# Optimization experiments

Measured on AMD Instinct MI355X. Metric: run time of the kernel, lower is better.

Reference implementation:

```python
import jax, jax.numpy as jnp
import numpy as np

# Dims: B=1, S=2048, D=1024, L=4 blocks, INNER=2*D=2048, NH=4 heads (DH=512),
# conv K=4, qkv blocksize BS=4 (NB=512 block-diagonal blocks).

def _ln(x, w, eps=1e-5):
    mu = x.mean(-1, keepdims=True)
    var = x.var(-1, keepdims=True)
    return (x - mu) * jax.lax.rsqrt(var + eps) * w


def setup_inputs() -> dict:
    key = jax.random.key(0)
    B, S, D = 1, 2048, 1024
    L, NH, K, BS = 4, 4, 4, 4
    INNER = 2 * D
    NB = INNER // BS
    ks = iter(jax.random.split(key, 40))
    rn = lambda *sh: jax.random.normal(next(ks), sh, jnp.float32) * 0.02
    return dict(
        tokens_batch=jax.random.normal(next(ks), (B, S, D), jnp.float32),
        ln_w=jnp.ones((L, D), jnp.float32),
        up_w=rn(L, 2 * INNER, D),
        conv_w=rn(L, INNER, K),
        conv_b=jnp.zeros((L, INNER), jnp.float32),
        q_w=rn(L, NB, BS, BS),
        k_w=rn(L, NB, BS, BS),
        v_w=rn(L, NB, BS, BS),
        ig_w=rn(L, NH, 3 * INNER),
        ig_b=jnp.zeros((L, NH), jnp.float32),
        fg_w=rn(L, NH, 3 * INNER),
        fg_b=jnp.tile(jnp.linspace(3.0, 6.0, NH, dtype=jnp.float32), (L, 1)),
        skip=jnp.ones((L, INNER), jnp.float32),
        onorm_w=jnp.ones((L, INNER), jnp.float32),
        down_w=rn(L, D, INNER),
        post_w=jnp.ones((D,), jnp.float32),
        lat_w=rn(32 * 32, D), lat_b=jnp.zeros((32 * 32,), jnp.float32),
        r1_w=rn(D, D), r1_b=jnp.zeros((D,), jnp.float32),
        r2_w=rn(1, D), r2_b=jnp.zeros((1,), jnp.float32),
        t1_w=rn(D, D), t1_b=jnp.zeros((D,), jnp.float32),
        t2_w=rn(1, D), t2_b=jnp.zeros((1,), jnp.float32),
    )


def reference(tokens_batch, ln_w, up_w, conv_w, conv_b, q_w, k_w, v_w,
              ig_w, ig_b, fg_w, fg_b, skip, onorm_w, down_w, post_w,
              lat_w, lat_b, r1_w, r1_b, r2_w, r2_b, t1_w, t1_b, t2_w, t2_b):
    B, S, D = tokens_batch.shape
    L, INNER, K = conv_w.shape
    NH = ig_w.shape[1]
    DH = INNER // NH
    NB, BS = q_w.shape[1], q_w.shape[2]
    mask = jnp.tril(jnp.ones((S, S), bool))
    x = tokens_batch
    for l in range(L):
        xn = _ln(x, ln_w[l])                                  # pre-LN (weight only)
        up = jnp.einsum('bsd,ed->bse', xn, up_w[l])           # (B,S,2*INNER)
        xm, z = up[..., :INNER], up[..., INNER:]
        # causal depthwise conv1d + swish
        xp = jnp.pad(xm, ((0, 0), (K - 1, 0), (0, 0)))
        xc = conv_b[l] + sum(xp[:, k:k + S, :] * conv_w[l, :, k] for k in range(K))
        xc = jax.nn.silu(xc)
        # block-diagonal (headwise) q/k/v projections
        def headwise(inp, w):
            return jnp.einsum('bsnd,nod->bsno', inp.reshape(B, S, NB, BS), w).reshape(B, S, INNER)
        q = headwise(xc, q_w[l]); kk = headwise(xc, k_w[l]); v = headwise(xm, v_w[l])
        gin = jnp.concatenate([q, kk, v], axis=-1)            # (B,S,3*INNER)
        ig = (jnp.einsum('bse,he->bsh', gin, ig_w[l]) + ig_b[l]).transpose(0, 2, 1)  # (B,NH,S)
        fg = (jnp.einsum('bse,he->bsh', gin, fg_w[l]) + fg_b[l]).transpose(0, 2, 1)
        qh = q.reshape(B, S, NH, DH).transpose(0, 2, 1, 3)
        kh = kk.reshape(B, S, NH, DH).transpose(0, 2, 1, 3)
        vh = v.reshape(B, S, NH, DH).transpose(0, 2, 1, 3)
        # parallel stabilized mLSTM (rowwise stabilization)
        cs = jnp.cumsum(jax.nn.log_sigmoid(fg), axis=-1)      # (B,NH,S)
        logD = jnp.where(mask, cs[..., :, None] - cs[..., None, :], -jnp.inf) + ig[:, :, None, :]
        m = jnp.max(logD, axis=-1, keepdims=True)
        Dm = jnp.exp(logD - m)
        qk = jnp.einsum('bhsd,bhtd->bhst', qh, kh) / jnp.sqrt(jnp.float32(DH))
        C = qk * Dm
        n = jnp.maximum(jnp.abs(C.sum(-1, keepdims=True)), jnp.exp(-m))
        h = jnp.einsum('bhst,bhtd->bhsd', C / (n + 1e-6), vh)
        # multi-head layernorm over DH per head, then channel scale
        ht = h.transpose(0, 2, 1, 3)                           # (B,S,NH,DH)
        mu = ht.mean(-1, keepdims=True); var = ht.var(-1, keepdims=True)
        ht = (ht - mu) * jax.lax.rsqrt(var + 1e-5) * onorm_w[l].reshape(NH, DH)
        ht = ht.reshape(B, S, INNER) + skip[l] * xc            # learnable skip
        out = ht * jax.nn.silu(z)                              # output gate
        x = x + jnp.einsum('bse,de->bsd', out, down_w[l])      # residual
    x = _ln(x, post_w)
    latent = jnp.einsum('bsd,ed->bse', x, lat_w) + lat_b
    reward = jnp.einsum('bsd,ed->bse', jnp.einsum('bsd,ed->bse', x, r1_w) + r1_b, r2_w) + r2_b
    term = jnp.einsum('bsd,ed->bse', jnp.einsum('bsd,ed->bse', x, t1_w) + t1_b, t2_w) + t2_b
    return (latent, reward, term)
```

## Files before the change

kernel.cpp:

```cpp
#include <hip/hip_runtime.h>
#include <hip/hip_bf16.h>
#include <math.h>
#include <cstdint>

typedef __bf16 bf16_t;
typedef bf16_t bf16x8 __attribute__((ext_vector_type(8)));
typedef bf16_t bf16x4 __attribute__((ext_vector_type(4)));
typedef bf16_t bf16x2 __attribute__((ext_vector_type(2)));
typedef float f32x4 __attribute__((ext_vector_type(4)));
typedef float f32x2 __attribute__((ext_vector_type(2)));

#define S_LEN 2048
#define DMODEL 1024
#define NLAYER 4
#define NHEAD 4
#define INNER 2048
#define DHEAD 512
#define NBLK 512
#define UPCOLS 4096
#define GIN 6144

#define GLDS16(gp, lp)                                              \
  __builtin_amdgcn_global_load_lds(                                 \
      (const __attribute__((address_space(1))) void*)(gp),          \
      (__attribute__((address_space(3))) void*)(lp), 16, 0, 0)

__global__ void zero_f32(float* __restrict__ p, int n) {
  int i = blockIdx.x * 256 + threadIdx.x;
  if (i < n) p[i] = 0.f;
}

__global__ __launch_bounds__(256) void cvt_f32_bf16(const float* __restrict__ in,
                                                    bf16_t* __restrict__ out, int n4) {
  int i = blockIdx.x * 256 + threadIdx.x;
  int stride = gridDim.x * 256;
  for (; i < n4; i += stride) {
    f32x4 v = ((const f32x4*)in)[i];
    bf16x4 o;
    #pragma unroll
    for (int j = 0; j < 4; j++) o[j] = (bf16_t)v[j];
    ((bf16x4*)out)[i] = o;
  }
}

__global__ __launch_bounds__(256) void ln_fused(const float* src, const float* p0,
                                                const float* p1, const float* __restrict__ w,
                                                float* Xout, bf16_t* __restrict__ out) {
  int s = blockIdx.x;
  int t = threadIdx.x;
  size_t base = (size_t)s * DMODEL;
  f32x4 v = ((const f32x4*)(src + base))[t];
  if (p0) {
    f32x4 a = ((const f32x4*)(p0 + base))[t];
    f32x4 b = ((const f32x4*)(p1 + base))[t];
    #pragma unroll
    for (int j = 0; j < 4; j++) v[j] += a[j] + b[j];
  }
  ((f32x4*)(Xout + base))[t] = v;
  float s1 = v[0] + v[1] + v[2] + v[3];
  float s2 = v[0]*v[0] + v[1]*v[1] + v[2]*v[2] + v[3]*v[3];
  __shared__ float b1[4], b2[4];
  #pragma unroll
  for (int off = 32; off; off >>= 1) { s1 += __shfl_xor(s1, off); s2 += __shfl_xor(s2, off); }
  if ((t & 63) == 0) { b1[t >> 6] = s1; b2[t >> 6] = s2; }
  __syncthreads();
  float tot1 = b1[0] + b1[1] + b1[2] + b1[3];
  float tot2 = b2[0] + b2[1] + b2[2] + b2[3];
  float mu = tot1 * (1.f / DMODEL);
  float var = tot2 * (1.f / DMODEL) - mu * mu;
  float rs = rsqrtf(var + 1e-5f);
  bf16x4 o;
  #pragma unroll
  for (int j = 0; j < 4; j++) o[j] = (bf16_t)((v[j] - mu) * rs * w[t * 4 + j]);
  ((bf16x4*)(out + base))[t] = o;
}

__global__ __launch_bounds__(256) void conv_qkv_kernel(
    const float* __restrict__ UP, const float* __restrict__ cw, const float* __restrict__ cb,
    const float* __restrict__ qw, const float* __restrict__ kw, const float* __restrict__ vw,
    float* __restrict__ XC, bf16_t* __restrict__ Q, bf16_t* __restrict__ Kb, bf16_t* __restrict__ V) {
  int s = blockIdx.y;
  int n = blockIdx.x * 256 + threadIdx.x;
  int c0 = n * 4;
  f32x4 zero4 = {};
  f32x4 xm[4];
  #pragma unroll
  for (int k = 0; k < 4; k++) {
    int sr = s + k - 3;
    xm[k] = (sr >= 0) ? *(const f32x4*)(UP + (size_t)sr * UPCOLS + c0) : zero4;
  }
  f32x4 cbv = *(const f32x4*)(cb + c0);
  float xc[4];
  #pragma unroll
  for (int d = 0; d < 4; d++) {
    f32x4 wv = *(const f32x4*)(cw + (size_t)(c0 + d) * 4);
    float a = cbv[d];
    #pragma unroll
    for (int k = 0; k < 4; k++) a += wv[k] * xm[k][d];
    xc[d] = a / (1.f + __expf(-a));
  }
  f32x4 xcv; xcv[0]=xc[0]; xcv[1]=xc[1]; xcv[2]=xc[2]; xcv[3]=xc[3];
  *(f32x4*)(XC + (size_t)s * INNER + c0) = xcv;
  bf16x4 qo, ko, vo;
  #pragma unroll
  for (int o = 0; o < 4; o++) {
    float aq = 0, ak = 0, av = 0;
    #pragma unroll
    for (int d = 0; d < 4; d++) {
      aq += qw[n * 16 + o * 4 + d] * xc[d];
      ak += kw[n * 16 + o * 4 + d] * xc[d];
      av += vw[n * 16 + o * 4 + d] * xm[3][d];
    }
    qo[o] = (bf16_t)aq; ko[o] = (bf16_t)ak; vo[o] = (bf16_t)av;
  }
  ((bf16x4*)(Q  + (size_t)s * INNER))[n] = qo;
  ((bf16x4*)(Kb + (size_t)s * INNER))[n] = ko;
  ((bf16x4*)(V  + (size_t)s * INNER))[n] = vo;
}

__global__ __launch_bounds__(256) void transpose_bf16(const bf16_t* __restrict__ in,
                                                      bf16_t* __restrict__ out) {
  __shared__ bf16_t tile[32][33];
  int c0 = blockIdx.x * 32, r0 = blockIdx.y * 32;
  int tx = threadIdx.x & 31, ty = threadIdx.x >> 5;
  #pragma unroll
  for (int i = ty; i < 32; i += 8) tile[i][tx] = in[(size_t)(r0 + i) * INNER + c0 + tx];
  __syncthreads();
  #pragma unroll
  for (int i = ty; i < 32; i += 8) out[(size_t)(c0 + i) * S_LEN + r0 + tx] = tile[tx][i];
}

__global__ __launch_bounds__(256) void gates_kernel(
    const bf16_t* __restrict__ Q, const bf16_t* __restrict__ K, const bf16_t* __restrict__ V,
    const float* __restrict__ igw, const float* __restrict__ igb,
    const float* __restrict__ fgw, const float* __restrict__ fgb,
    float* __restrict__ IG, float* __restrict__ FG) {
  int s = blockIdx.x;
  float pi[NHEAD] = {0, 0, 0, 0}, pf[NHEAD] = {0, 0, 0, 0};
  for (int e = threadIdx.x; e < GIN; e += 256) {
    float g;
    if (e < INNER)            g = (float)Q[(size_t)s * INNER + e];
    else if (e < 2 * INNER)   g = (float)K[(size_t)s * INNER + e - INNER];
    else                      g = (float)V[(size_t)s * INNER + e - 2 * INNER];
    #pragma unroll
    for (int h = 0; h < NHEAD; h++) {
      pi[h] += g * igw[h * GIN + e];
      pf[h] += g * fgw[h * GIN + e];
    }
  }
  __shared__ float red[8][4];
  #pragma unroll
  for (int h = 0; h < NHEAD; h++) {
    float a = pi[h], b = pf[h];
    #pragma unroll
    for (int off = 32; off; off >>= 1) { a += __shfl_xor(a, off); b += __shfl_xor(b, off); }
    if ((threadIdx.x & 63) == 0) { red[h][threadIdx.x >> 6] = a; red[h + 4][threadIdx.x >> 6] = b; }
  }
  __syncthreads();
  if (threadIdx.x < NHEAD) {
    int h = threadIdx.x;
    IG[h * S_LEN + s] = red[h][0] + red[h][1] + red[h][2] + red[h][3] + igb[h];
    FG[h * S_LEN + s] = red[h + 4][0] + red[h + 4][1] + red[h + 4][2] + red[h + 4][3] + fgb[h];
  }
}

__global__ __launch_bounds__(256) void scan_kernel(const float* __restrict__ IG,
                                                   const float* __restrict__ FG,
                                                   float* __restrict__ AV, float* __restrict__ PM,
                                                   float* __restrict__ NF) {
  int h = blockIdx.x;
  int tid = threadIdx.x;
  const float* fg = FG + h * S_LEN;
  const float* ig = IG + h * S_LEN;
  float cs[8];
  float run = 0.f;
  #pragma unroll
  for (int i = 0; i < 8; i++) {
    float x = fg[tid * 8 + i];
    float l = (x >= 0.f) ? -log1pf(__expf(-x)) : (x - log1pf(__expf(x)));
    run += l; cs[i] = run;
  }
  __shared__ float sb[256];
  sb[tid] = run;
  __syncthreads();
  for (int off = 1; off < 256; off <<= 1) {
    float add = (tid >= off) ? sb[tid - off] : 0.f;
    __syncthreads();
    sb[tid] += add;
    __syncthreads();
  }
  float base = sb[tid] - run;
  float a[8];
  float runm = -__builtin_inff();
  #pragma unroll
  for (int i = 0; i < 8; i++) {
    cs[i] += base;
    a[i] = ig[tid * 8 + i] - cs[i];
    runm = fmaxf(runm, a[i]);
  }
  __syncthreads();
  sb[tid] = runm;
  __syncthreads();
  for (int off = 1; off < 256; off <<= 1) {
    float other = (tid >= off) ? sb[tid - off] : -__builtin_inff();
    __syncthreads();
    sb[tid] = fmaxf(sb[tid], other);
    __syncthreads();
  }
  float rm = (tid == 0) ? -__builtin_inff() : sb[tid - 1];
  #pragma unroll
  for (int i = 0; i < 8; i++) {
    rm = fmaxf(rm, a[i]);
    AV[h * S_LEN + tid * 8 + i] = a[i];
    PM[h * S_LEN + tid * 8 + i] = rm;
    NF[h * S_LEN + tid * 8 + i] = __expf(-(cs[i] + rm));
  }
}

__global__ void scale_kernel(const float* __restrict__ nraw, const float* __restrict__ nf,
                             float* __restrict__ scale, int n) {
  int i = blockIdx.x * 256 + threadIdx.x;
  if (i < n) scale[i] = 1.f / (fmaxf(fabsf(nraw[i]), nf[i]) + 1e-6f);
}

__global__ __launch_bounds__(256) void onorm_kernel(
    const float* __restrict__ Hp0, const float* __restrict__ Hp1,
    const float* __restrict__ XC, const float* __restrict__ UP,
    const float* __restrict__ onw, const float* __restrict__ skipw, bf16_t* __restrict__ OUT) {
  int h = blockIdx.x, s = blockIdx.y;
  int c = h * DHEAD + threadIdx.x * 2;
  size_t idx = (size_t)s * INNER + c;
  f32x2 v0 = *(const f32x2*)(Hp0 + idx);
  f32x2 v1 = *(const f32x2*)(Hp1 + idx);
  f32x2 v; v[0] = v0[0] + v1[0]; v[1] = v0[1] + v1[1];
  float s1 = v[0] + v[1], s2 = v[0] * v[0] + v[1] * v[1];
  __shared__ float b1[4], b2[4];
  #pragma unroll
  for (int off = 32; off; off >>= 1) { s1 += __shfl_xor(s1, off); s2 += __shfl_xor(s2, off); }
  if ((threadIdx.x & 63) == 0) { b1[threadIdx.x >> 6] = s1; b2[threadIdx.x >> 6] = s2; }
  __syncthreads();
  float tot1 = b1[0] + b1[1] + b1[2] + b1[3];
  float tot2 = b2[0] + b2[1] + b2[2] + b2[3];
  float mu = tot1 * (1.f / DHEAD);
  float var = tot2 * (1.f / DHEAD) - mu * mu;
  float rs = rsqrtf(var + 1e-5f);
  bf16x2 o;
  #pragma unroll
  for (int j = 0; j < 2; j++) {
    float val = (v[j] - mu) * rs * onw[c + j] + skipw[c + j] * XC[idx + j];
    float z = UP[(size_t)s * UPCOLS + INNER + c + j];
    val *= z / (1.f + __expf(-z));
    o[j] = (bf16_t)val;
  }
  *(bf16x2*)(OUT + idx) = o;
}

__global__ __launch_bounds__(256) void latcopy_kernel(const float* __restrict__ Ch,
                                                      const float* __restrict__ b,
                                                      float* __restrict__ out) {
  int s = blockIdx.x, t = threadIdx.x;
  f32x4 v = ((const f32x4*)(Ch + (size_t)s * 3072))[t];
  f32x4 bb = ((const f32x4*)b)[t];
  f32x4 o; o[0]=v[0]+bb[0]; o[1]=v[1]+bb[1]; o[2]=v[2]+bb[2]; o[3]=v[3]+bb[3];
  ((f32x4*)(out + (size_t)s * DMODEL))[t] = o;
}

__global__ __launch_bounds__(256) void rt_kernel(
    const float* __restrict__ Ch,
    const float* __restrict__ r1b, const float* __restrict__ t1b,
    const float* __restrict__ r2w, const float* __restrict__ r2b,
    const float* __restrict__ t2w, const float* __restrict__ t2b,
    float* __restrict__ outR, float* __restrict__ outT) {
  int s = blockIdx.x, t = threadIdx.x;
  f32x4 a = ((const f32x4*)(Ch + (size_t)s * 3072 + 1024))[t];
  f32x4 b = ((const f32x4*)(Ch + (size_t)s * 3072 + 2048))[t];
  f32x4 ab = ((const f32x4*)r1b)[t];
  f32x4 bb = ((const f32x4*)t1b)[t];
  f32x4 w1 = ((const f32x4*)r2w)[t];
  f32x4 w2 = ((const f32x4*)t2w)[t];
  float pr = 0, pt = 0;
  #pragma unroll
  for (int j = 0; j < 4; j++) {
    pr += (a[j] + ab[j]) * w1[j];
    pt += (b[j] + bb[j]) * w2[j];
  }
  __shared__ float rb[4], tb[4];
  #pragma unroll
  for (int off = 32; off; off >>= 1) { pr += __shfl_xor(pr, off); pt += __shfl_xor(pt, off); }
  if ((t & 63) == 0) { rb[t >> 6] = pr; tb[t >> 6] = pt; }
  __syncthreads();
  if (t == 0) {
    outR[s] = rb[0] + rb[1] + rb[2] + rb[3] + r2b[0];
    outT[s] = tb[0] + tb[1] + tb[2] + tb[3] + t2b[0];
  }
}

#define BM 128
#define BN 128

template <int MODE>
__global__ __launch_bounds__(256) void gemm_kernel(
    const bf16_t* __restrict__ A, int lda, long long sAz,
    const bf16_t* __restrict__ B, int ldb, long long sBz,
    float* __restrict__ C, int ldc, long long sCz,
    bf16_t* __restrict__ P, long long sPz,
    int K,
    const float* __restrict__ avec, const float* __restrict__ pmvec,
    float* __restrict__ nraw,
    const float* __restrict__ scalev, long long sVz) {
  int gx = gridDim.x, gxy = gx * gridDim.y;
  int nwg = gxy * gridDim.z;
  int orig = blockIdx.z * gxy + blockIdx.y * gx + blockIdx.x;
  int xcd = orig & 7, lo = orig >> 3;
  int q8 = nwg >> 3, r8 = nwg & 7;
  int wg = (xcd < r8 ? xcd * (q8 + 1) : r8 * (q8 + 1) + (xcd - r8) * q8) + lo;
  int z = wg / gxy; int rem = wg - z * gxy;
  int by, bx;
  if (MODE == 3) {
    by = (int)((sqrtf(8.f * (float)rem + 1.f) - 1.f) * 0.5f);
    while ((by + 1) * (by + 2) / 2 <= rem) by++;
    while (by * (by + 1) / 2 > rem) by--;
    bx = rem - by * (by + 1) / 2;
  } else {
    by = rem / gx; bx = rem - by * gx;
  }
  int m0 = by * BM;
  int n0 = bx * BN;

  int head = z, kbeg = 0, kend = K;
  if (MODE == 4) {
    head = z >> 1;
    int kf = m0 + BM; if (kf > K) kf = K;
    int half = kf >> 1;
    kbeg = (z & 1) * half; kend = kbeg + half;
    A += (size_t)head * sAz; B += (size_t)head * sBz;
  } else if (MODE == 6) {
    head = 0;
    int half = K >> 1;
    kbeg = z * half; kend = kbeg + half;
  } else {
    A += (size_t)z * sAz; B += (size_t)z * sBz;
  }
  int nt = (kend - kbeg) >> 5;

  constexpr int SME = (MODE == 3) ? (128 * 136) : 16384;
  __shared__ __align__(16) bf16_t smem[SME];

  int tid = threadIdx.x;
  int lane = tid & 63;
  int wave = tid >> 6;
  int wr = wave >> 1, wc = wave & 1;
  int l15 = lane & 15, lk = lane >> 4;

  int csw = ((lane & 3) ^ ((lane >> 3) & 3)) * 8;
  const bf16_t* pA0 = A + (size_t)(m0 + wave * 32 + (lane >> 2)) * lda + kbeg + csw;
  const bf16_t* pA1 = pA0 + (size_t)16 * lda;
  const bf16_t* pB0 = B + (size_t)(n0 + wave * 32 + (lane >> 2)) * ldb + kbeg + csw;
  const bf16_t* pB1 = pB0 + (size_t)16 * ldb;
  bf16_t* ldsA = smem + wave * 1024;
  bf16_t* ldsB = smem + 4096 + wave * 1024;

#define STAGE(t, db)                                   \
  do {                                                 \
    int _ko = (t) * 32;                                \
    bf16_t* _ba = ldsA + (db) * 8192;                  \
    bf16_t* _bb = ldsB + (db) * 8192;                  \
    GLDS16(pA0 + _ko, _ba);                            \
    GLDS16(pA1 + _ko, _ba + 512);                      \
    GLDS16(pB0 + _ko, _bb);                            \
    GLDS16(pB1 + _ko, _bb + 512);                      \
  } while (0)

  int aoff[4], boff[4];
  #pragma unroll
  for (int m = 0; m < 4; m++) {
    int ra = wr * 64 + m * 16 + l15;
    aoff[m] = ra * 64 + ((lk ^ ((ra >> 1) & 3)) * 16);
    int rb = wc * 64 + m * 16 + l15;
    boff[m] = 8192 + rb * 64 + ((lk ^ ((rb >> 1) & 3)) * 16);
  }

  f32x4 acc[4][4] = {};

  STAGE(0, 0);
  asm volatile("s_waitcnt vmcnt(0)" ::: "memory");
  __builtin_amdgcn_s_barrier();
  int cur = 0;
  for (int t = 0; t < nt; ++t) {
    if (t + 1 < nt) STAGE(t + 1, cur ^ 1);
    __builtin_amdgcn_sched_barrier(0);
    const char* base = (const char*)smem + cur * 16384;
    bf16x8 af[4], bfv[4];
    #pragma unroll
    for (int m = 0; m < 4; m++) af[m] = *(const bf16x8*)(base + aoff[m]);
    #pragma unroll
    for (int n = 0; n < 4; n++) bfv[n] = *(const bf16x8*)(base + boff[n]);
    asm volatile("s_waitcnt lgkmcnt(0)" ::: "memory");
    __builtin_amdgcn_sched_barrier(0);
    __builtin_amdgcn_s_setprio(1);
    #pragma unroll
    for (int m = 0; m < 4; m++)
      #pragma unroll
      for (int n = 0; n < 4; n++)
        acc[m][n] = __builtin_amdgcn_mfma_f32_16x16x32_bf16(af[m], bfv[n], acc[m][n], 0, 0, 0);
    __builtin_amdgcn_s_setprio(0);
    asm volatile("s_waitcnt vmcnt(0)" ::: "memory");
    __builtin_amdgcn_s_barrier();
    cur ^= 1;
  }
#undef STAGE

  int rbase = m0 + wr * 64;
  int cbase = n0 + wc * 64;
  if (MODE == 3) {
    const float* av = avec + z * sVz;
    const float* pv = pmvec + z * sVz;
    float* nr = nraw + z * sVz;
    bf16_t* Pp = P + z * sPz;
    const float ISQ = 0.04419417382415922f;
    #pragma unroll
    for (int m = 0; m < 4; m++) {
      float rsum[4] = {0, 0, 0, 0};
      #pragma unroll
      for (int n = 0; n < 4; n++) {
        int cg = cbase + n * 16 + l15;
        float aexp = av[cg];
        #pragma unroll
        for (int r = 0; r < 4; r++) {
          int rg = rbase + m * 16 + lk * 4 + r;
          float val = 0.f;
          if (cg <= rg) val = acc[m][n][r] * ISQ * __expf(aexp - pv[rg]);
          smem[(size_t)(wr * 64 + m * 16 + lk * 4 + r) * 136 + wc * 64 + n * 16 + l15] =
              (bf16_t)val;
          rsum[r] += val;
        }
      }
      #pragma unroll
      for (int r = 0; r < 4; r++) {
        float v = rsum[r];
        v += __shfl_xor(v, 1); v += __shfl_xor(v, 2); v += __shfl_xor(v, 4); v += __shfl_xor(v, 8);
        if (l15 == 0) atomicAdd(&nr[rbase + m * 16 + lk * 4 + r], v);
      }
    }
    __syncthreads();
    #pragma unroll
    for (int i = 0; i < 8; i++) {
      int chunk = tid + i * 256;
      int row = chunk >> 4, cc = chunk & 15;
      *(bf16x8*)(Pp + (size_t)(m0 + row) * ldc + n0 + cc * 8) =
          *(const bf16x8*)(smem + (size_t)row * 136 + cc * 8);
    }
  } else {
    float* Cp = C;
    if (MODE == 4) Cp = C + (size_t)head * sCz + (size_t)(z & 1) * sPz;
    else if (MODE == 6) Cp = C + (size_t)z * sPz;
    else Cp = C + (size_t)head * sCz;
    #pragma unroll
    for (int m = 0; m < 4; m++) {
      #pragma unroll
      for (int r = 0; r < 4; r++) {
        int rg = rbase + m * 16 + lk * 4 + r;
        float rowscale = (MODE == 4) ? scalev[head * sVz + rg] : 1.f;
        #pragma unroll
        for (int n = 0; n < 4; n++) {
          int cg = cbase + n * 16 + l15;
          size_t idx = (size_t)rg * ldc + cg;
          float v = acc[m][n][r];
          if (MODE == 4) Cp[idx] = v * rowscale;
          else Cp[idx] = v;
        }
      }
    }
  }
}

extern "C" void kernel_launch(void* const* d_in, const int* in_sizes, int n_in,
                              void* d_out, int out_size, void* d_ws, size_t ws_size,
                              hipStream_t stream) {
  const float* tokens = (const float*)d_in[0];
  const float* ln_w   = (const float*)d_in[1];
  const float* up_w   = (const float*)d_in[2];
  const float* conv_w = (const float*)d_in[3];
  const float* conv_b = (const float*)d_in[4];
  const float* q_w    = (const float*)d_in[5];
  const float* k_w    = (const float*)d_in[6];
  const float* v_w    = (const float*)d_in[7];
  const float* ig_w   = (const float*)d_in[8];
  const float* ig_b   = (const float*)d_in[9];
  const float* fg_w   = (const float*)d_in[10];
  const float* fg_b   = (const float*)d_in[11];
  const float* skipw  = (const float*)d_in[12];
  const float* onormw = (const float*)d_in[13];
  const float* down_w = (const float*)d_in[14];
  const float* post_w = (const float*)d_in[15];
  const float* lat_w  = (const float*)d_in[16];
  const float* lat_b  = (const float*)d_in[17];
  const float* r1_w   = (const float*)d_in[18];
  const float* r1_b   = (const float*)d_in[19];
  const float* r2_w   = (const float*)d_in[20];
  const float* r2_b   = (const float*)d_in[21];
  const float* t1_w   = (const float*)d_in[22];
  const float* t1_b   = (const float*)d_in[23];
  const float* t2_w   = (const float*)d_in[24];
  const float* t2_b   = (const float*)d_in[25];

  char* ws = (char*)d_ws;
  size_t off = 0;
  auto alloc = [&](size_t bytes) -> char* {
    char* p = ws + off;
    off += (bytes + 255) & ~(size_t)255;
    return p;
  };
  float*  X    = (float*)alloc((size_t)S_LEN * DMODEL * 4);
  float*  UP   = (float*)alloc((size_t)S_LEN * UPCOLS * 4);
  float*  XC   = (float*)alloc((size_t)S_LEN * INNER * 4);
  float*  Hp0  = (float*)alloc((size_t)S_LEN * INNER * 4);
  float*  Hp1  = (float*)alloc((size_t)S_LEN * INNER * 4);
  bf16_t* XN   = (bf16_t*)alloc((size_t)S_LEN * DMODEL * 2);
  bf16_t* Qb   = (bf16_t*)alloc((size_t)S_LEN * INNER * 2);
  bf16_t* Kb   = (bf16_t*)alloc((size_t)S_LEN * INNER * 2);
  bf16_t* Vb   = (bf16_t*)alloc((size_t)S_LEN * INNER * 2);
  bf16_t* VT   = (bf16_t*)alloc((size_t)S_LEN * INNER * 2);
  bf16_t* Pb   = (bf16_t*)alloc((size_t)NHEAD * S_LEN * S_LEN * 2);
  bf16_t* OUTb = (bf16_t*)alloc((size_t)S_LEN * INNER * 2);
  bf16_t* Wb   = (bf16_t*)alloc((size_t)UPCOLS * DMODEL * 2);
  bf16_t* Wb2  = (bf16_t*)alloc((size_t)DMODEL * INNER * 2);
  float*  IG   = (float*)alloc(NHEAD * S_LEN * 4);
  float*  FG   = (float*)alloc(NHEAD * S_LEN * 4);
  float*  AV   = (float*)alloc(NHEAD * S_LEN * 4);
  float*  PM   = (float*)alloc(NHEAD * S_LEN * 4);
  float*  NF   = (float*)alloc(NHEAD * S_LEN * 4);
  float*  NRAW = (float*)alloc(NHEAD * S_LEN * 4);
  float*  SCL  = (float*)alloc(NHEAD * S_LEN * 4);
  float* Dp0 = Hp0;
  float* Dp1 = Hp0 + (size_t)S_LEN * DMODEL;
  float* Chead = UP;
  float* latent_out = (float*)d_out;
  float* reward_out = (float*)d_out + (size_t)S_LEN * DMODEL;
  float* term_out   = reward_out + S_LEN;

  if (off > ws_size) return;

  for (int l = 0; l < NLAYER; l++) {
    ln_fused<<<S_LEN, 256, 0, stream>>>(l == 0 ? tokens : X, l == 0 ? nullptr : Dp0,
                                        l == 0 ? nullptr : Dp1, ln_w + l * DMODEL, X, XN);
    cvt_f32_bf16<<<1024, 256, 0, stream>>>(up_w + (size_t)l * UPCOLS * DMODEL, Wb,
                                           UPCOLS * DMODEL / 4);
    gemm_kernel<0><<<dim3(UPCOLS / BN, S_LEN / BM, 1), 256, 0, stream>>>(
        XN, DMODEL, 0, Wb, DMODEL, 0, UP, UPCOLS, 0, nullptr, 0,
        DMODEL, nullptr, nullptr, nullptr, nullptr, 0);
    conv_qkv_kernel<<<dim3(2, S_LEN), 256, 0, stream>>>(
        UP, conv_w + (size_t)l * INNER * 4, conv_b + l * INNER,
        q_w + (size_t)l * NBLK * 16, k_w + (size_t)l * NBLK * 16, v_w + (size_t)l * NBLK * 16,
        XC, Qb, Kb, Vb);
    transpose_bf16<<<dim3(64, 64), 256, 0, stream>>>(Vb, VT);
    gates_kernel<<<S_LEN, 256, 0, stream>>>(Qb, Kb, Vb, ig_w + (size_t)l * NHEAD * GIN,
                                            ig_b + l * NHEAD, fg_w + (size_t)l * NHEAD * GIN,
                                            fg_b + l * NHEAD, IG, FG);
    scan_kernel<<<NHEAD, 256, 0, stream>>>(IG, FG, AV, PM, NF);
    zero_f32<<<(NHEAD * S_LEN + 255) / 256, 256, 0, stream>>>(NRAW, NHEAD * S_LEN);
    gemm_kernel<3><<<dim3(136, 1, NHEAD), 256, 0, stream>>>(
        Qb, INNER, DHEAD, Kb, INNER, DHEAD, nullptr, S_LEN, 0, Pb, (long long)S_LEN * S_LEN,
        DHEAD, AV, PM, NRAW, nullptr, S_LEN);
    scale_kernel<<<(NHEAD * S_LEN + 255) / 256, 256, 0, stream>>>(NRAW, NF, SCL, NHEAD * S_LEN);
    gemm_kernel<4><<<dim3(DHEAD / BN, S_LEN / BM, 2 * NHEAD), 256, 0, stream>>>(
        Pb, S_LEN, (long long)S_LEN * S_LEN, VT, S_LEN, (long long)DHEAD * S_LEN,
        Hp0, INNER, DHEAD, nullptr, (long long)S_LEN * INNER,
        S_LEN, nullptr, nullptr, nullptr, SCL, S_LEN);
    onorm_kernel<<<dim3(NHEAD, S_LEN), 256, 0, stream>>>(Hp0, Hp1, XC, UP, onormw + l * INNER,
                                                         skipw + l * INNER, OUTb);
    cvt_f32_bf16<<<1024, 256, 0, stream>>>(down_w + (size_t)l * DMODEL * INNER, Wb2,
                                           DMODEL * INNER / 4);
    gemm_kernel<6><<<dim3(DMODEL / BN, S_LEN / BM, 2), 256, 0, stream>>>(
        OUTb, INNER, 0, Wb2, INNER, 0, Dp0, DMODEL, 0, nullptr, (long long)S_LEN * DMODEL,
        INNER, nullptr, nullptr, nullptr, nullptr, 0);
  }

  ln_fused<<<S_LEN, 256, 0, stream>>>(X, Dp0, Dp1, post_w, X, XN);
  bf16_t* Wh = Wb;
  cvt_f32_bf16<<<512, 256, 0, stream>>>(lat_w, Wh, DMODEL * DMODEL / 4);
  cvt_f32_bf16<<<512, 256, 0, stream>>>(r1_w, Wh + (size_t)DMODEL * DMODEL, DMODEL * DMODEL / 4);
  cvt_f32_bf16<<<512, 256, 0, stream>>>(t1_w, Wh + 2 * (size_t)DMODEL * DMODEL,
                                        DMODEL * DMODEL / 4);
  gemm_kernel<0><<<dim3(3072 / BN, S_LEN / BM, 1), 256, 0, stream>>>(
      XN, DMODEL, 0, Wh, DMODEL, 0, Chead, 3072, 0, nullptr, 0,
      DMODEL, nullptr, nullptr, nullptr, nullptr, 0);
  latcopy_kernel<<<S_LEN, 256, 0, stream>>>(Chead, lat_b, latent_out);
  rt_kernel<<<S_LEN, 256, 0, stream>>>(Chead, r1_b, t1_b, r2_w, r2_b, t2_w, t2_b,
                                       reward_out, term_out);
}
```

Before: 962.1 us.

## Deepen GEMM pipeline to 4-stage LDS ring and hoist weight conversions

The GEMM main loop moves from a double-buffered scheme with two barriers per k-step to a 4-slot LDS ring with three tiles prefetched. It uses graded vmcnt waits and one barrier per iteration, aiming to hide global-load latency better. All bf16 weight conversions are hoisted into a few up-front launches, and zeroing NRAW is folded into the scan kernel, removing per-layer launches. LDS use per block rises to 64KB for every mode, which may lower occupancy.

```diff
diff --git a/kernel.cpp b/kernel.cpp
--- a/kernel.cpp
+++ b/kernel.cpp
@@ -24,11 +24,6 @@
   __builtin_amdgcn_global_load_lds(                                 \
       (const __attribute__((address_space(1))) void*)(gp),          \
       (__attribute__((address_space(3))) void*)(lp), 16, 0, 0)
-
-__global__ void zero_f32(float* __restrict__ p, int n) {
-  int i = blockIdx.x * 256 + threadIdx.x;
-  if (i < n) p[i] = 0.f;
-}
 
 __global__ __launch_bounds__(256) void cvt_f32_bf16(const float* __restrict__ in,
                                                     bf16_t* __restrict__ out, int n4) {
@@ -167,7 +162,7 @@
 __global__ __launch_bounds__(256) void scan_kernel(const float* __restrict__ IG,
                                                    const float* __restrict__ FG,
                                                    float* __restrict__ AV, float* __restrict__ PM,
-                                                   float* __restrict__ NF) {
+                                                   float* __restrict__ NF, float* __restrict__ NRAW) {
   int h = blockIdx.x;
   int tid = threadIdx.x;
   const float* fg = FG + h * S_LEN;
@@ -214,6 +209,7 @@
     AV[h * S_LEN + tid * 8 + i] = a[i];
     PM[h * S_LEN + tid * 8 + i] = rm;
     NF[h * S_LEN + tid * 8 + i] = __expf(-(cs[i] + rm));
+    NRAW[h * S_LEN + tid * 8 + i] = 0.f;
   }
 }
 
@@ -343,8 +339,7 @@
   }
   int nt = (kend - kbeg) >> 5;
 
-  constexpr int SME = (MODE == 3) ? (128 * 136) : 16384;
-  __shared__ __align__(16) bf16_t smem[SME];
+  __shared__ __align__(16) bf16_t smem[32768];
 
   int tid = threadIdx.x;
   int lane = tid & 63;
@@ -357,18 +352,15 @@
   const bf16_t* pA1 = pA0 + (size_t)16 * lda;
   const bf16_t* pB0 = B + (size_t)(n0 + wave * 32 + (lane >> 2)) * ldb + kbeg + csw;
   const bf16_t* pB1 = pB0 + (size_t)16 * ldb;
-  bf16_t* ldsA = smem + wave * 1024;
-  bf16_t* ldsB = smem + 4096 + wave * 1024;
-
-#define STAGE(t, db)                                   \
+
+#define STAGE(t)                                       \
   do {                                                 \
     int _ko = (t) * 32;                                \
-    bf16_t* _ba = ldsA + (db) * 8192;                  \
-    bf16_t* _bb = ldsB + (db) * 8192;                  \
-    GLDS16(pA0 + _ko, _ba);                            \
-    GLDS16(pA1 + _ko, _ba + 512);                      \
-    GLDS16(pB0 + _ko, _bb);                            \
-    GLDS16(pB1 + _ko, _bb + 512);                      \
+    bf16_t* _b = smem + ((t) & 3) * 8192 + wave * 1024;\
+    GLDS16(pA0 + _ko, _b);                             \
+    GLDS16(pA1 + _ko, _b + 512);                       \
+    GLDS16(pB0 + _ko, _b + 4096);                      \
+    GLDS16(pB1 + _ko, _b + 4096 + 512);                \
   } while (0)
 
   int aoff[4], boff[4];
@@ -382,14 +374,17 @@
 
   f32x4 acc[4][4] = {};
 
-  STAGE(0, 0);
-  asm volatile("s_waitcnt vmcnt(0)" ::: "memory");
-  __builtin_amdgcn_s_barrier();
-  int cur = 0;
+  int npre = nt < 3 ? nt : 3;
+  for (int s = 0; s < npre; ++s) STAGE(s);
+
   for (int t = 0; t < nt; ++t) {
-    if (t + 1 < nt) STAGE(t + 1, cur ^ 1);
-    __builtin_amdgcn_sched_barrier(0);
-    const char* base = (const char*)smem + cur * 16384;
+    int remt = nt - 1 - t;
+    if (remt >= 2)      asm volatile("s_waitcnt vmcnt(8)" ::: "memory");
+    else if (remt == 1) asm volatile("s_waitcnt vmcnt(4)" ::: "memory");
+    else                asm volatile("s_waitcnt vmcnt(0)" ::: "memory");
+    __builtin_amdgcn_s_barrier();
+    if (t + 3 < nt) STAGE(t + 3);
+    const char* base = (const char*)smem + (t & 3) * 16384;
     bf16x8 af[4], bfv[4];
     #pragma unroll
     for (int m = 0; m < 4; m++) af[m] = *(const bf16x8*)(base + aoff[m]);
@@ -404,15 +399,13 @@
       for (int n = 0; n < 4; n++)
         acc[m][n] = __builtin_amdgcn_mfma_f32_16x16x32_bf16(af[m], bfv[n], acc[m][n], 0, 0, 0);
     __builtin_amdgcn_s_setprio(0);
-    asm volatile("s_waitcnt vmcnt(0)" ::: "memory");
-    __builtin_amdgcn_s_barrier();
-    cur ^= 1;
   }
 #undef STAGE
 
   int rbase = m0 + wr * 64;
   int cbase = n0 + wc * 64;
   if (MODE == 3) {
+    __syncthreads();
     const float* av = avec + z * sVz;
     const float* pv = pmvec + z * sVz;
     float* nr = nraw + z * sVz;
@@ -523,8 +516,9 @@
   bf16_t* VT   = (bf16_t*)alloc((size_t)S_LEN * INNER * 2);
   bf16_t* Pb   = (bf16_t*)alloc((size_t)NHEAD * S_LEN * S_LEN * 2);
   bf16_t* OUTb = (bf16_t*)alloc((size_t)S_LEN * INNER * 2);
-  bf16_t* Wb   = (bf16_t*)alloc((size_t)UPCOLS * DMODEL * 2);
-  bf16_t* Wb2  = (bf16_t*)alloc((size_t)DMODEL * INNER * 2);
+  bf16_t* WbU  = (bf16_t*)alloc((size_t)NLAYER * UPCOLS * DMODEL * 2);
+  bf16_t* WbD  = (bf16_t*)alloc((size_t)NLAYER * DMODEL * INNER * 2);
+  bf16_t* Wh   = (bf16_t*)alloc((size_t)3 * DMODEL * DMODEL * 2);
   float*  IG   = (float*)alloc(NHEAD * S_LEN * 4);
   float*  FG   = (float*)alloc(NHEAD * S_LEN * 4);
   float*  AV   = (float*)alloc(NHEAD * S_LEN * 4);
@@ -541,13 +535,18 @@
 
   if (off > ws_size) return;
 
+  cvt_f32_bf16<<<2048, 256, 0, stream>>>(up_w, WbU, NLAYER * UPCOLS * DMODEL / 4);
+  cvt_f32_bf16<<<1024, 256, 0, stream>>>(down_w, WbD, NLAYER * DMODEL * INNER / 4);
+  cvt_f32_bf16<<<512, 256, 0, stream>>>(lat_w, Wh, DMODEL * DMODEL / 4);
+  cvt_f32_bf16<<<512, 256, 0, stream>>>(r1_w, Wh + (size_t)DMODEL * DMODEL, DMODEL * DMODEL / 4);
+  cvt_f32_bf16<<<512, 256, 0, stream>>>(t1_w, Wh + 2 * (size_t)DMODEL * DMODEL,
+                                        DMODEL * DMODEL / 4);
+
   for (int l = 0; l < NLAYER; l++) {
     ln_fused<<<S_LEN, 256, 0, stream>>>(l == 0 ? tokens : X, l == 0 ? nullptr : Dp0,
                                         l == 0 ? nullptr : Dp1, ln_w + l * DMODEL, X, XN);
-    cvt_f32_bf16<<<1024, 256, 0, stream>>>(up_w + (size_t)l * UPCOLS * DMODEL, Wb,
-                                           UPCOLS * DMODEL / 4);
     gemm_kernel<0><<<dim3(UPCOLS / BN, S_LEN / BM, 1), 256, 0, stream>>>(
-        XN, DMODEL, 0, Wb, DMODEL, 0, UP, UPCOLS, 0, nullptr, 0,
+        XN, DMODEL, 0, WbU + (size_t)l * UPCOLS * DMODEL, DMODEL, 0, UP, UPCOLS, 0, nullptr, 0,
         DMODEL, nullptr, nullptr, nullptr, nullptr, 0);
     conv_qkv_kernel<<<dim3(2, S_LEN), 256, 0, stream>>>(
         UP, conv_w + (size_t)l * INNER * 4, conv_b + l * INNER,
@@ -557,8 +556,7 @@
     gates_kernel<<<S_LEN, 256, 0, stream>>>(Qb, Kb, Vb, ig_w + (size_t)l * NHEAD * GIN,
                                             ig_b + l * NHEAD, fg_w + (size_t)l * NHEAD * GIN,
                                             fg_b + l * NHEAD, IG, FG);
-    scan_kernel<<<NHEAD, 256, 0, stream>>>(IG, FG, AV, PM, NF);
-    zero_f32<<<(NHEAD * S_LEN + 255) / 256, 256, 0, stream>>>(NRAW, NHEAD * S_LEN);
+    scan_kernel<<<NHEAD, 256, 0, stream>>>(IG, FG, AV, PM, NF, NRAW);
     gemm_kernel<3><<<dim3(136, 1, NHEAD), 256, 0, stream>>>(
         Qb, INNER, DHEAD, Kb, INNER, DHEAD, nullptr, S_LEN, 0, Pb, (long long)S_LEN * S_LEN,
         DHEAD, AV, PM, NRAW, nullptr, S_LEN);
@@ -569,19 +567,12 @@
         S_LEN, nullptr, nullptr, nullptr, SCL, S_LEN);
     onorm_kernel<<<dim3(NHEAD, S_LEN), 256, 0, stream>>>(Hp0, Hp1, XC, UP, onormw + l * INNER,
                                                          skipw + l * INNER, OUTb);
-    cvt_f32_bf16<<<1024, 256, 0, stream>>>(down_w + (size_t)l * DMODEL * INNER, Wb2,
-                                           DMODEL * INNER / 4);
     gemm_kernel<6><<<dim3(DMODEL / BN, S_LEN / BM, 2), 256, 0, stream>>>(
-        OUTb, INNER, 0, Wb2, INNER, 0, Dp0, DMODEL, 0, nullptr, (long long)S_LEN * DMODEL,
-        INNER, nullptr, nullptr, nullptr, nullptr, 0);
+        OUTb, INNER, 0, WbD + (size_t)l * DMODEL * INNER, INNER, 0, Dp0, DMODEL, 0, nullptr,
+        (long long)S_LEN * DMODEL, INNER, nullptr, nullptr, nullptr, nullptr, 0);
   }
 
   ln_fused<<<S_LEN, 256, 0, stream>>>(X, Dp0, Dp1, post_w, X, XN);
-  bf16_t* Wh = Wb;
-  cvt_f32_bf16<<<512, 256, 0, stream>>>(lat_w, Wh, DMODEL * DMODEL / 4);
-  cvt_f32_bf16<<<512, 256, 0, stream>>>(r1_w, Wh + (size_t)DMODEL * DMODEL, DMODEL * DMODEL / 4);
-  cvt_f32_bf16<<<512, 256, 0, stream>>>(t1_w, Wh + 2 * (size_t)DMODEL * DMODEL,
-                                        DMODEL * DMODEL / 4);
   gemm_kernel<0><<<dim3(3072 / BN, S_LEN / BM, 1), 256, 0, stream>>>(
       XN, DMODEL, 0, Wh, DMODEL, 0, Chead, 3072, 0, nullptr, 0,
       DMODEL, nullptr, nullptr, nullptr, nullptr, 0);
```

Result: no change. 977.7 us (+1.6%).
